# Kernel optimization log

Hardware: AMD Instinct MI355X
Metric: run time of the kernel (lower is better)

The kernel has to match this reference:

```python
import jax, jax.numpy as jnp
import numpy as np

N = 100000
E = 1600000
H = 64      # hidden_size
NH = 8      # num_heads
DH = H // NH  # per-head dim (heads are the LAST axis, as in the torch code)


def _lin(x, W, b):
    return x @ W + b


def setup_inputs() -> dict:
    key = jax.random.key(0)
    ks = jax.random.split(key, 18)
    s = 0.05
    inp = {
        "h_x": jax.random.normal(ks[0], (N, H), jnp.float32),
        "h_e": jax.random.normal(ks[1], (E, H), jnp.float32),
        "row": jax.random.randint(ks[2], (E,), 0, N, jnp.int32),  # dst node of each nonzero
        "col": jax.random.randint(ks[3], (E,), 0, N, jnp.int32),  # src node of each nonzero
    }
    names = ["q", "k", "v", "e", "oh", "oe"]
    for i, nm in enumerate(names):
        inp["W" + nm] = jax.random.normal(ks[4 + 2 * i], (H, H), jnp.float32) * s
        inp["b" + nm] = jax.random.normal(ks[5 + 2 * i], (H,), jnp.float32) * s
    return inp


def reference(h_x, h_e, row, col, Wq, bq, Wk, bk, Wv, bv, We, be, Woh, boh, Woe, boe):
    n = h_x.shape[0]
    m = h_e.shape[0]
    q = _lin(h_x, Wq, bq).reshape(n, DH, NH)
    k = _lin(h_x, Wk, bk).reshape(n, DH, NH)
    v = _lin(h_x, Wv, bv).reshape(n, DH, NH)
    e = _lin(h_e, We, be).reshape(m, DH, NH)

    # SDDMM: per-nonzero (i=row, j=col), per-head dot of q[i] and k[j]  -> (E, NH)
    scores = (q[row] * k[col]).sum(axis=1) / jnp.sqrt(jnp.float32(DH))

    # edge gating: e.sum over dh axis -> (E, NH)
    e_gate = e.sum(axis=1)
    scores = scores * e_gate

    # oe branch (uses pre-softmax gated scores)
    oe_feat = scores[:, None, :] * e          # (E, DH, NH)
    oe = _lin(oe_feat.reshape(m, H), Woe, boe)

    # sparse softmax over dim=1 (per destination row), per head
    mx = jax.ops.segment_max(scores, row, num_segments=n)      # (N, NH)
    ex = jnp.exp(scores - mx[row])
    den = jax.ops.segment_sum(ex, row, num_segments=n)         # (N, NH)
    sm = ex / den[row]                                          # (E, NH)

    # bSpMM: h_out[i,:,h] = sum_{e: row[e]=i} sm[e,h] * v[col[e],:,h]
    h_out = jax.ops.segment_sum(sm[:, None, :] * v[col], row, num_segments=n)
    oh = _lin(h_out.reshape(n, H), Woh, boh)
    return (oh, oe)
```

## Files before the change

kernel.cpp:

```cpp
#include <hip/hip_runtime.h>

typedef __attribute__((ext_vector_type(8))) short bf16x8;
typedef __attribute__((ext_vector_type(4))) float f32x4;
typedef __attribute__((ext_vector_type(16))) unsigned char u8x16;

__device__ __forceinline__ float bf2f(unsigned short h) {
  return __uint_as_float(((unsigned)h) << 16);
}
__device__ __forceinline__ unsigned cvtpk(float a, float b) {
  unsigned r;
  asm("v_cvt_pk_bf16_f32 %0, %1, %2" : "=v"(r) : "v"(a), "v"(b));
  return r;
}
__device__ __forceinline__ unsigned short f2bf(float f) {
  return (unsigned short)(cvtpk(f, f) & 0xffffu);
}
__device__ __forceinline__ bf16x8 pack8(f32x4 x0, f32x4 x1) {
  union { bf16x8 v; unsigned u[4]; } z;
  z.u[0] = cvtpk(x0[0], x0[1]);
  z.u[1] = cvtpk(x0[2], x0[3]);
  z.u[2] = cvtpk(x1[0], x1[1]);
  z.u[3] = cvtpk(x1[2], x1[3]);
  return z.v;
}

__device__ __forceinline__ int fragpos(int nb, int n15) {
  return (((nb & 1) * 2 + (n15 >> 3)) << 4) + ((nb >> 1) << 3) + (n15 & 7);
}

template<bool IN_BF16, bool OUT_BF16>
__global__ void __launch_bounds__(256) gemm64_kernel(const void* __restrict__ Ain,
    const float* __restrict__ W, const float* __restrict__ bias,
    void* __restrict__ Out, int M) {
  const int tid = threadIdx.x;
  const int l = tid & 63;
  const int g = l >> 4;
  const int n15 = l & 15;

  bf16x8 bfrag[4][2];
  float bv[4];
#pragma unroll
  for (int nb = 0; nb < 4; ++nb) {
    bv[nb] = bias[nb * 16 + n15];
#pragma unroll
    for (int kb = 0; kb < 2; ++kb)
#pragma unroll
      for (int j = 0; j < 8; ++j)
        bfrag[nb][kb][j] = (short)f2bf(W[(kb * 32 + g * 8 + j) * 64 + nb * 16 + n15]);
  }

  int wid = (blockIdx.x * blockDim.x + tid) >> 6;
  int nw = (gridDim.x * blockDim.x) >> 6;
  int ntiles = (M + 15) >> 4;
  for (int t = wid; t < ntiles; t += nw) {
    int m0 = t << 4;
    int arow = m0 + n15;
    bf16x8 a0, a1;
    if (arow < M) {
      if constexpr (IN_BF16) {
        const unsigned short* ap = (const unsigned short*)Ain + (size_t)arow * 64 + g * 8;
        a0 = *(const bf16x8*)ap;
        a1 = *(const bf16x8*)(ap + 32);
      } else {
        const float* ap = (const float*)Ain + (size_t)arow * 64 + g * 8;
        a0 = pack8(*(const f32x4*)ap, *(const f32x4*)(ap + 4));
        a1 = pack8(*(const f32x4*)(ap + 32), *(const f32x4*)(ap + 36));
      }
    } else {
#pragma unroll
      for (int j = 0; j < 8; ++j) { a0[j] = 0; a1[j] = 0; }
    }
    f32x4 acc[4];
#pragma unroll
    for (int nb = 0; nb < 4; ++nb) {
      acc[nb] = (f32x4){bv[nb], bv[nb], bv[nb], bv[nb]};
      acc[nb] = __builtin_amdgcn_mfma_f32_16x16x32_bf16(a0, bfrag[nb][0], acc[nb], 0, 0, 0);
      acc[nb] = __builtin_amdgcn_mfma_f32_16x16x32_bf16(a1, bfrag[nb][1], acc[nb], 0, 0, 0);
    }
#pragma unroll
    for (int nb = 0; nb < 4; ++nb)
#pragma unroll
      for (int r = 0; r < 4; ++r) {
        int orow = m0 + g * 4 + r;
        if (orow < M) {
          float val = acc[nb][r];
          size_t oidx = (size_t)orow * 64 + nb * 16 + n15;
          if constexpr (OUT_BF16) ((unsigned short*)Out)[oidx] = f2bf(val);
          else                    ((float*)Out)[oidx] = val;
        }
      }
  }
}

__global__ void __launch_bounds__(256) qkv3_kernel(const float* __restrict__ hx,
    const float* __restrict__ Wq, const float* __restrict__ bq,
    const float* __restrict__ Wk, const float* __restrict__ bk,
    const float* __restrict__ Wv, const float* __restrict__ bv,
    signed char* __restrict__ q8, signed char* __restrict__ k8,
    signed char* __restrict__ v8,
    float* __restrict__ sq, float* __restrict__ sk, float* __restrict__ sv, int M) {
  const int tid = threadIdx.x;
  const int l = tid & 63;
  const int g = l >> 4;
  const int n15 = l & 15;
  const float* Ws[3] = {Wq, Wk, Wv};
  const float* bs[3] = {bq, bk, bv};
  signed char* outs[3] = {q8, k8, v8};
  float* scl[3] = {sq, sk, sv};

  bf16x8 bfrag[3][4][2];
  float bvv[3][4];
#pragma unroll
  for (int w = 0; w < 3; ++w)
#pragma unroll
    for (int nb = 0; nb < 4; ++nb) {
      bvv[w][nb] = bs[w][nb * 16 + n15];
#pragma unroll
      for (int kb = 0; kb < 2; ++kb)
#pragma unroll
        for (int j = 0; j < 8; ++j)
          bfrag[w][nb][kb][j] = (short)f2bf(Ws[w][(kb * 32 + g * 8 + j) * 64 + nb * 16 + n15]);
    }

  int wid = (blockIdx.x * blockDim.x + tid) >> 6;
  int nw = (gridDim.x * blockDim.x) >> 6;
  int ntiles = (M + 15) >> 4;
  for (int t = wid; t < ntiles; t += nw) {
    int m0 = t << 4;
    int arow = m0 + n15;
    bf16x8 a0, a1;
    if (arow < M) {
      const float* ap = hx + (size_t)arow * 64 + g * 8;
      a0 = pack8(*(const f32x4*)ap, *(const f32x4*)(ap + 4));
      a1 = pack8(*(const f32x4*)(ap + 32), *(const f32x4*)(ap + 36));
    } else {
#pragma unroll
      for (int j = 0; j < 8; ++j) { a0[j] = 0; a1[j] = 0; }
    }
#pragma unroll
    for (int w = 0; w < 3; ++w) {
      f32x4 acc[4];
#pragma unroll
      for (int nb = 0; nb < 4; ++nb) {
        acc[nb] = (f32x4){bvv[w][nb], bvv[w][nb], bvv[w][nb], bvv[w][nb]};
        acc[nb] = __builtin_amdgcn_mfma_f32_16x16x32_bf16(a0, bfrag[w][nb][0], acc[nb], 0, 0, 0);
        acc[nb] = __builtin_amdgcn_mfma_f32_16x16x32_bf16(a1, bfrag[w][nb][1], acc[nb], 0, 0, 0);
      }
#pragma unroll
      for (int r = 0; r < 4; ++r) {
        float am = fmaxf(fmaxf(fabsf(acc[0][r]), fabsf(acc[1][r])),
                         fmaxf(fabsf(acc[2][r]), fabsf(acc[3][r])));
        am = fmaxf(am, __shfl_xor(am, 1, 64));
        am = fmaxf(am, __shfl_xor(am, 2, 64));
        am = fmaxf(am, __shfl_xor(am, 4, 64));
        am = fmaxf(am, __shfl_xor(am, 8, 64));
        am = fmaxf(am, 1e-10f);
        float inv = 127.0f / am;
        int orow = m0 + g * 4 + r;
        if (orow < M) {
          if (n15 == 0) scl[w][orow] = am / 127.0f;
#pragma unroll
          for (int nb = 0; nb < 4; ++nb) {
            int qi = __float2int_rn(acc[nb][r] * inv);
            int pos = (w == 2) ? (nb * 16 + n15) : fragpos(nb, n15);
            outs[w][(size_t)orow * 64 + pos] = (signed char)qi;
          }
        }
      }
    }
  }
}

__global__ void wemprep_kernel(const float* __restrict__ We, const float* __restrict__ be,
                               float* __restrict__ WeM, float* __restrict__ beM) {
  int tid = threadIdx.x;
  if (tid < 512) {
    int d = tid >> 3, h = tid & 7;
    float s = 0.f;
#pragma unroll
    for (int m = 0; m < 8; ++m) s += We[d * 64 + m * 8 + h];
    WeM[d * 8 + h] = s * 0.35355339059327373f;
  }
  if (tid < 8) {
    float s = 0.f;
#pragma unroll
    for (int m = 0; m < 8; ++m) s += be[tid + m * 8];
    beM[tid] = s * 0.35355339059327373f;
  }
}

__global__ void __launch_bounds__(256) edge_fused_kernel(
    const float* __restrict__ he,
    const int* __restrict__ rowi, const int* __restrict__ coli,
    const int* __restrict__ eslot,
    const signed char* __restrict__ q8, const signed char* __restrict__ k8,
    const float* __restrict__ sq, const float* __restrict__ sk,
    const float* __restrict__ We, const float* __restrict__ be,
    const float* __restrict__ Woe, const float* __restrict__ boe,
    const float* __restrict__ WeM, const float* __restrict__ beM,
    float* __restrict__ oe, float* __restrict__ escores, int E) {
  const int tid = threadIdx.x;
  const int wv = tid >> 6;
  const int l = tid & 63;
  const int g = l >> 4;
  const int n15 = l & 15;

  __shared__ unsigned short feat_lds[4][16 * 72];

  bf16x8 bfE[4][2], bfO[4][2];
  float beV[4], boV[4];
#pragma unroll
  for (int nb = 0; nb < 4; ++nb) {
    beV[nb] = be[nb * 16 + n15];
    boV[nb] = boe[nb * 16 + n15];
#pragma unroll
    for (int kb = 0; kb < 2; ++kb)
#pragma unroll
      for (int j = 0; j < 8; ++j) {
        bfE[nb][kb][j] = (short)f2bf(We[(kb * 32 + g * 8 + j) * 64 + nb * 16 + n15]);
        bfO[nb][kb][j] = (short)f2bf(Woe[(kb * 32 + g * 8 + j) * 64 + nb * 16 + n15]);
      }
  }
  bf16x8 gB0, gB1, mB;
  const bool hv = (n15 < 8);
#pragma unroll
  for (int j = 0; j < 8; ++j) {
    gB0[j] = hv ? (short)f2bf(WeM[(g * 8 + j) * 8 + n15]) : (short)0;
    gB1[j] = hv ? (short)f2bf(WeM[(32 + g * 8 + j) * 8 + n15]) : (short)0;
    mB[j]  = (hv && j == n15) ? (short)0x3F80 : (short)0;
  }
  const float beMv = hv ? beM[n15] : 0.f;

  const int ntiles = (E + 15) >> 4;
  int wid = (blockIdx.x * blockDim.x + tid) >> 6;
  int nw = (gridDim.x * blockDim.x) >> 6;
  for (int t = wid; t < ntiles; t += nw) {
    const int m0 = t << 4;
    const int es = min(m0 + n15, E - 1);
    const int rq = rowi[es], rc = coli[es], sl = eslot[es];

    u8x16 qv = *(const u8x16*)(q8 + (size_t)rq * 64 + g * 16);
    u8x16 kv = *(const u8x16*)(k8 + (size_t)rc * 64 + g * 16);
    const float sqk = sq[rq] * sk[rc];

    const float* ap = he + (size_t)es * 64 + g * 8;
    bf16x8 a0 = pack8(*(const f32x4*)ap, *(const f32x4*)(ap + 4));
    bf16x8 a1 = pack8(*(const f32x4*)(ap + 32), *(const f32x4*)(ap + 36));

    f32x4 acc[4];
#pragma unroll
    for (int nb = 0; nb < 4; ++nb) {
      acc[nb] = (f32x4){beV[nb], beV[nb], beV[nb], beV[nb]};
      acc[nb] = __builtin_amdgcn_mfma_f32_16x16x32_bf16(a0, bfE[nb][0], acc[nb], 0, 0, 0);
      acc[nb] = __builtin_amdgcn_mfma_f32_16x16x32_bf16(a1, bfE[nb][1], acc[nb], 0, 0, 0);
    }
    f32x4 gate = (f32x4){beMv, beMv, beMv, beMv};
    gate = __builtin_amdgcn_mfma_f32_16x16x32_bf16(a0, gB0, gate, 0, 0, 0);
    gate = __builtin_amdgcn_mfma_f32_16x16x32_bf16(a1, gB1, gate, 0, 0, 0);

    f32x4 p0a, p0b, p1a, p1b;
#pragma unroll
    for (int j = 0; j < 4; ++j) {
      p0a[j] = (float)((int)(signed char)qv[j]      * (int)(signed char)kv[j]);
      p0b[j] = (float)((int)(signed char)qv[4 + j]  * (int)(signed char)kv[4 + j]);
      p1a[j] = (float)((int)(signed char)qv[8 + j]  * (int)(signed char)kv[8 + j]);
      p1b[j] = (float)((int)(signed char)qv[12 + j] * (int)(signed char)kv[12 + j]);
    }
    bf16x8 pa0 = pack8(p0a, p0b), pa1 = pack8(p1a, p1b);
    f32x4 p = (f32x4){0.f, 0.f, 0.f, 0.f};
    p = __builtin_amdgcn_mfma_f32_16x16x32_bf16(pa0, mB, p, 0, 0, 0);
    p = __builtin_amdgcn_mfma_f32_16x16x32_bf16(pa1, mB, p, 0, 0, 0);

    float s_[4];
#pragma unroll
    for (int r = 0; r < 4; ++r)
      s_[r] = p[r] * gate[r] * __shfl(sqk, g * 4 + r, 64);
#pragma unroll
    for (int r = 0; r < 4; ++r) {
      int slot = __shfl(sl, g * 4 + r, 64);
      if (hv && m0 + g * 4 + r < E) escores[(size_t)slot * 8 + n15] = s_[r];
    }
#pragma unroll
    for (int r = 0; r < 4; ++r) {
      float o = __shfl_xor(s_[r], 8, 64);
      if (!hv) s_[r] = o;
    }
#pragma unroll
    for (int nb = 0; nb < 4; ++nb)
#pragma unroll
      for (int r = 0; r < 4; ++r)
        feat_lds[wv][(g * 4 + r) * 72 + nb * 16 + n15] = f2bf(s_[r] * acc[nb][r]);
    const unsigned short* fpt = &feat_lds[wv][n15 * 72 + g * 8];
    a0 = *(const bf16x8*)fpt;
    a1 = *(const bf16x8*)(fpt + 32);
#pragma unroll
    for (int nb = 0; nb < 4; ++nb) {
      f32x4 c2 = (f32x4){boV[nb], boV[nb], boV[nb], boV[nb]};
      c2 = __builtin_amdgcn_mfma_f32_16x16x32_bf16(a0, bfO[nb][0], c2, 0, 0, 0);
      c2 = __builtin_amdgcn_mfma_f32_16x16x32_bf16(a1, bfO[nb][1], c2, 0, 0, 0);
#pragma unroll
      for (int r = 0; r < 4; ++r) {
        int orow = m0 + g * 4 + r;
        if (orow < E) oe[(size_t)orow * 64 + nb * 16 + n15] = c2[r];
      }
    }
  }
}

__global__ void zero_kernel(int* __restrict__ p, int n) {
  int i = blockIdx.x * blockDim.x + threadIdx.x;
  if (i < n) p[i] = 0;
}

__global__ void hist_kernel(const int* __restrict__ row, int* __restrict__ deg, int E) {
  int gid = blockIdx.x * blockDim.x + threadIdx.x;
  if (gid < E) atomicAdd(&deg[row[gid]], 1);
}

#define SCAN_B 256
#define SCAN_E 8
__global__ void scan1_kernel(const int* __restrict__ deg, int* __restrict__ rowptr,
                             int* __restrict__ blksum, int n) {
  __shared__ int sh[SCAN_B];
  int base = blockIdx.x * (SCAN_B * SCAN_E) + threadIdx.x * SCAN_E;
  int v[SCAN_E];
  int s = 0;
#pragma unroll
  for (int j = 0; j < SCAN_E; ++j) {
    v[j] = (base + j < n) ? deg[base + j] : 0;
    s += v[j];
  }
  sh[threadIdx.x] = s;
  __syncthreads();
  for (int off = 1; off < SCAN_B; off <<= 1) {
    int t = (threadIdx.x >= off) ? sh[threadIdx.x - off] : 0;
    __syncthreads();
    sh[threadIdx.x] += t;
    __syncthreads();
  }
  if (threadIdx.x == SCAN_B - 1) blksum[blockIdx.x] = sh[SCAN_B - 1];
  int run = sh[threadIdx.x] - s;
#pragma unroll
  for (int j = 0; j < SCAN_E; ++j) {
    if (base + j < n) rowptr[base + j] = run;
    run += v[j];
  }
}

__global__ void scan2_kernel(int* __restrict__ blksum, int nb) {
  __shared__ int sh[SCAN_B];
  int v = (threadIdx.x < nb) ? blksum[threadIdx.x] : 0;
  sh[threadIdx.x] = v;
  __syncthreads();
  for (int off = 1; off < SCAN_B; off <<= 1) {
    int t = (threadIdx.x >= off) ? sh[threadIdx.x - off] : 0;
    __syncthreads();
    sh[threadIdx.x] += t;
    __syncthreads();
  }
  if (threadIdx.x < nb) blksum[threadIdx.x] = sh[threadIdx.x] - v;
}

__global__ void scan3_kernel(int* __restrict__ rowptr, int* __restrict__ cursor,
                             const int* __restrict__ blksum, int n) {
  int i = blockIdx.x * blockDim.x + threadIdx.x;
  if (i >= n) return;
  int v = rowptr[i] + blksum[i / (SCAN_B * SCAN_E)];
  rowptr[i] = v;
  cursor[i] = v;
}

__global__ void scatter_kernel(const int* __restrict__ row, const int* __restrict__ col,
                               int* __restrict__ cursor, int* __restrict__ eslot,
                               int* __restrict__ ecol, int E) {
  int gid = blockIdx.x * blockDim.x + threadIdx.x;
  if (gid >= E) return;
  int r = row[gid];
  int slot = atomicAdd(&cursor[r], 1);
  eslot[gid] = slot;
  ecol[slot] = col[gid];
}

__global__ void __launch_bounds__(256) row_attn_kernel(const float* __restrict__ escores,
    const int* __restrict__ rowptr, const int* __restrict__ deg,
    const int* __restrict__ ecol,
    const signed char* __restrict__ v8, const float* __restrict__ sv,
    float* __restrict__ hout, int n) {
  int gid = blockIdx.x * blockDim.x + threadIdx.x;
  int r = gid >> 6, lane = threadIdx.x & 63;
  if (r >= n) return;
  int gi = lane >> 4, j = lane & 15;
  int start = rowptr[r], dg = deg[r];

  f32x4 acc = (f32x4){0.f, 0.f, 0.f, 0.f};
  f32x4 den = (f32x4){0.f, 0.f, 0.f, 0.f};
  for (int i = gi; i < dg; i += 4) {
    int idx = start + i;
    int c = ecol[idx];
    f32x4 svec = *(const f32x4*)(escores + (size_t)idx * 8 + 4 * (j & 1));
    unsigned vvu = *(const unsigned*)(v8 + (size_t)c * 64 + j * 4);
    float scv = sv[c];
#pragma unroll
    for (int m = 0; m < 4; ++m) {
      float ex = __expf(svec[m]);
      float vm = (float)((signed char)((vvu >> (8 * m)) & 0xff));
      den[m] += ex;
      acc[m] += ex * scv * vm;
    }
  }
#pragma unroll
  for (int m = 0; m < 4; ++m) {
    acc[m] += __shfl_xor(acc[m], 16, 64);
    acc[m] += __shfl_xor(acc[m], 32, 64);
    den[m] += __shfl_xor(den[m], 16, 64);
    den[m] += __shfl_xor(den[m], 32, 64);
  }
  if (gi == 0) {
    f32x4 o;
#pragma unroll
    for (int m = 0; m < 4; ++m) o[m] = (dg > 0) ? acc[m] / den[m] : 0.f;
    *(f32x4*)(hout + (size_t)r * 64 + j * 4) = o;
  }
}

extern "C" void kernel_launch(void* const* d_in, const int* in_sizes, int n_in,
                              void* d_out, int out_size, void* d_ws, size_t ws_size,
                              hipStream_t stream) {
  const float* hx  = (const float*)d_in[0];
  const float* he  = (const float*)d_in[1];
  const int*   row = (const int*)d_in[2];
  const int*   col = (const int*)d_in[3];
  const float* Wq = (const float*)d_in[4],  *bq = (const float*)d_in[5];
  const float* Wk = (const float*)d_in[6],  *bk = (const float*)d_in[7];
  const float* Wv = (const float*)d_in[8],  *bv = (const float*)d_in[9];
  const float* We = (const float*)d_in[10], *be = (const float*)d_in[11];
  const float* Woh = (const float*)d_in[12], *boh = (const float*)d_in[13];
  const float* Woe = (const float*)d_in[14], *boe = (const float*)d_in[15];

  const int n = in_sizes[0] / 64;
  const int E = in_sizes[2];

  float* out = (float*)d_out;
  float* oh = out;
  float* oe = out + (size_t)n * 64;

  signed char* q8 = (signed char*)d_ws;
  signed char* k8 = q8 + (size_t)n * 64;
  signed char* v8 = k8 + (size_t)n * 64;
  float* sq = (float*)(v8 + (size_t)n * 64);
  float* sk = sq + n;
  float* sv = sk + n;
  float* escores = sv + n;
  float* hout    = escores + (size_t)E * 8;

  int* deg    = (int*)(hout + (size_t)n * 64);
  int* rowptr = deg + n;
  int* cursor = rowptr + n;
  int* blksum = cursor + n;
  int* eslot  = blksum + 256;
  int* ecol   = eslot + (size_t)E;
  float* WeM  = (float*)(ecol + (size_t)E);
  float* beM  = WeM + 512;

  const int nb_scan = (n + SCAN_B * SCAN_E - 1) / (SCAN_B * SCAN_E);

  zero_kernel<<<(n + 255) / 256, 256, 0, stream>>>(deg, n);
  hist_kernel<<<(E + 255) / 256, 256, 0, stream>>>(row, deg, E);
  scan1_kernel<<<nb_scan, SCAN_B, 0, stream>>>(deg, rowptr, blksum, n);
  scan2_kernel<<<1, SCAN_B, 0, stream>>>(blksum, nb_scan);
  scan3_kernel<<<(n + 255) / 256, 256, 0, stream>>>(rowptr, cursor, blksum, n);
  scatter_kernel<<<(E + 255) / 256, 256, 0, stream>>>(row, col, cursor, eslot, ecol, E);

  qkv3_kernel<<<512, 256, 0, stream>>>(hx, Wq, bq, Wk, bk, Wv, bv,
                                       q8, k8, v8, sq, sk, sv, n);
  wemprep_kernel<<<1, 512, 0, stream>>>(We, be, WeM, beM);

  edge_fused_kernel<<<2048, 256, 0, stream>>>(he, row, col, eslot, q8, k8, sq, sk,
                                              We, be, Woe, boe, WeM, beM,
                                              oe, escores, E);

  row_attn_kernel<<<(n + 3) / 4, 256, 0, stream>>>(escores, rowptr, deg, ecol,
                                                   v8, sv, hout, n);
  gemm64_kernel<false, false><<<512, 256, 0, stream>>>(hout, Woh, boh, oh, n);
}
```

Baseline: 596.3 us.

## Switch q/k/v from int8 to bf16 and software-pipeline edge gathers

Replaces per-row int8 quantization of q, k and v (with scale arrays) by plain bf16 storage. This removes the quantize reductions and scale loads but doubles the bytes gathered per edge. The edge kernel now prefetches the next tile's indices and q/k rows, two tiles ahead for indices, to hide gather latency at the cost of extra registers. The row attention loop is unrolled by two so more gather loads are in flight.

```diff
diff --git a/kernel.cpp b/kernel.cpp
--- a/kernel.cpp
+++ b/kernel.cpp
@@ -2,7 +2,7 @@
 
 typedef __attribute__((ext_vector_type(8))) short bf16x8;
 typedef __attribute__((ext_vector_type(4))) float f32x4;
-typedef __attribute__((ext_vector_type(16))) unsigned char u8x16;
+typedef __attribute__((ext_vector_type(4))) unsigned short u16x4;
 
 __device__ __forceinline__ float bf2f(unsigned short h) {
   return __uint_as_float(((unsigned)h) << 16);
@@ -22,10 +22,6 @@
   z.u[2] = cvtpk(x1[0], x1[1]);
   z.u[3] = cvtpk(x1[2], x1[3]);
   return z.v;
-}
-
-__device__ __forceinline__ int fragpos(int nb, int n15) {
-  return (((nb & 1) * 2 + (n15 >> 3)) << 4) + ((nb >> 1) << 3) + (n15 & 7);
 }
 
 template<bool IN_BF16, bool OUT_BF16>
@@ -96,17 +92,15 @@
     const float* __restrict__ Wq, const float* __restrict__ bq,
     const float* __restrict__ Wk, const float* __restrict__ bk,
     const float* __restrict__ Wv, const float* __restrict__ bv,
-    signed char* __restrict__ q8, signed char* __restrict__ k8,
-    signed char* __restrict__ v8,
-    float* __restrict__ sq, float* __restrict__ sk, float* __restrict__ sv, int M) {
+    unsigned short* __restrict__ q, unsigned short* __restrict__ k,
+    unsigned short* __restrict__ v, int M) {
   const int tid = threadIdx.x;
   const int l = tid & 63;
   const int g = l >> 4;
   const int n15 = l & 15;
   const float* Ws[3] = {Wq, Wk, Wv};
   const float* bs[3] = {bq, bk, bv};
-  signed char* outs[3] = {q8, k8, v8};
-  float* scl[3] = {sq, sk, sv};
+  unsigned short* outs[3] = {q, k, v};
 
   bf16x8 bfrag[3][4][2];
   float bvv[3][4];
@@ -147,26 +141,13 @@
         acc[nb] = __builtin_amdgcn_mfma_f32_16x16x32_bf16(a1, bfrag[w][nb][1], acc[nb], 0, 0, 0);
       }
 #pragma unroll
-      for (int r = 0; r < 4; ++r) {
-        float am = fmaxf(fmaxf(fabsf(acc[0][r]), fabsf(acc[1][r])),
-                         fmaxf(fabsf(acc[2][r]), fabsf(acc[3][r])));
-        am = fmaxf(am, __shfl_xor(am, 1, 64));
-        am = fmaxf(am, __shfl_xor(am, 2, 64));
-        am = fmaxf(am, __shfl_xor(am, 4, 64));
-        am = fmaxf(am, __shfl_xor(am, 8, 64));
-        am = fmaxf(am, 1e-10f);
-        float inv = 127.0f / am;
-        int orow = m0 + g * 4 + r;
-        if (orow < M) {
-          if (n15 == 0) scl[w][orow] = am / 127.0f;
-#pragma unroll
-          for (int nb = 0; nb < 4; ++nb) {
-            int qi = __float2int_rn(acc[nb][r] * inv);
-            int pos = (w == 2) ? (nb * 16 + n15) : fragpos(nb, n15);
-            outs[w][(size_t)orow * 64 + pos] = (signed char)qi;
-          }
+      for (int nb = 0; nb < 4; ++nb)
+#pragma unroll
+        for (int r = 0; r < 4; ++r) {
+          int orow = m0 + g * 4 + r;
+          if (orow < M)
+            outs[w][(size_t)orow * 64 + nb * 16 + n15] = f2bf(acc[nb][r]);
         }
-      }
     }
   }
 }
@@ -193,8 +174,7 @@
     const float* __restrict__ he,
     const int* __restrict__ rowi, const int* __restrict__ coli,
     const int* __restrict__ eslot,
-    const signed char* __restrict__ q8, const signed char* __restrict__ k8,
-    const float* __restrict__ sq, const float* __restrict__ sk,
+    const unsigned short* __restrict__ qb, const unsigned short* __restrict__ kbuf,
     const float* __restrict__ We, const float* __restrict__ be,
     const float* __restrict__ Woe, const float* __restrict__ boe,
     const float* __restrict__ WeM, const float* __restrict__ beM,
@@ -234,16 +214,47 @@
   const int ntiles = (E + 15) >> 4;
   int wid = (blockIdx.x * blockDim.x + tid) >> 6;
   int nw = (gridDim.x * blockDim.x) >> 6;
-  for (int t = wid; t < ntiles; t += nw) {
-    const int m0 = t << 4;
-    const int es = min(m0 + n15, E - 1);
-    const int rq = rowi[es], rc = coli[es], sl = eslot[es];
-
-    u8x16 qv = *(const u8x16*)(q8 + (size_t)rq * 64 + g * 16);
-    u8x16 kv = *(const u8x16*)(k8 + (size_t)rc * 64 + g * 16);
-    const float sqk = sq[rq] * sk[rc];
-
-    const float* ap = he + (size_t)es * 64 + g * 8;
+  if (wid >= ntiles) return;
+
+  int t0 = wid;
+  int sl0;
+  bf16x8 qv0, qv1, kv0, kv1;
+  {
+    int es = min((t0 << 4) + n15, E - 1);
+    int rq = rowi[es], rc = coli[es];
+    sl0 = eslot[es];
+    const unsigned short* qp = qb + (size_t)rq * 64 + g * 8;
+    const unsigned short* kp = kbuf + (size_t)rc * 64 + g * 8;
+    qv0 = *(const bf16x8*)qp; qv1 = *(const bf16x8*)(qp + 32);
+    kv0 = *(const bf16x8*)kp; kv1 = *(const bf16x8*)(kp + 32);
+  }
+  int t1 = t0 + nw;
+  bool more = t1 < ntiles;
+  int rq1 = 0, rc1 = 0, sl1 = 0;
+  if (more) {
+    int es = min((t1 << 4) + n15, E - 1);
+    rq1 = rowi[es]; rc1 = coli[es]; sl1 = eslot[es];
+  }
+
+  for (;;) {
+    bf16x8 nqv0 = qv0, nqv1 = qv1, nkv0 = kv0, nkv1 = kv1;
+    if (more) {
+      const unsigned short* qp = qb + (size_t)rq1 * 64 + g * 8;
+      const unsigned short* kp = kbuf + (size_t)rc1 * 64 + g * 8;
+      nqv0 = *(const bf16x8*)qp; nqv1 = *(const bf16x8*)(qp + 32);
+      nkv0 = *(const bf16x8*)kp; nkv1 = *(const bf16x8*)(kp + 32);
+    }
+    int t2 = t1 + nw;
+    bool more2 = more && (t2 < ntiles);
+    int rq2 = rq1, rc2 = rc1, sl2 = sl1;
+    if (more2) {
+      int es = min((t2 << 4) + n15, E - 1);
+      rq2 = rowi[es]; rc2 = coli[es]; sl2 = eslot[es];
+    }
+
+    const int m0 = t0 << 4;
+    const int es0 = min(m0 + n15, E - 1);
+    const float* ap = he + (size_t)es0 * 64 + g * 8;
     bf16x8 a0 = pack8(*(const f32x4*)ap, *(const f32x4*)(ap + 4));
     bf16x8 a1 = pack8(*(const f32x4*)(ap + 32), *(const f32x4*)(ap + 36));
 
@@ -261,10 +272,10 @@
     f32x4 p0a, p0b, p1a, p1b;
 #pragma unroll
     for (int j = 0; j < 4; ++j) {
-      p0a[j] = (float)((int)(signed char)qv[j]      * (int)(signed char)kv[j]);
-      p0b[j] = (float)((int)(signed char)qv[4 + j]  * (int)(signed char)kv[4 + j]);
-      p1a[j] = (float)((int)(signed char)qv[8 + j]  * (int)(signed char)kv[8 + j]);
-      p1b[j] = (float)((int)(signed char)qv[12 + j] * (int)(signed char)kv[12 + j]);
+      p0a[j] = bf2f((unsigned short)qv0[j]) * bf2f((unsigned short)kv0[j]);
+      p0b[j] = bf2f((unsigned short)qv0[4 + j]) * bf2f((unsigned short)kv0[4 + j]);
+      p1a[j] = bf2f((unsigned short)qv1[j]) * bf2f((unsigned short)kv1[j]);
+      p1b[j] = bf2f((unsigned short)qv1[4 + j]) * bf2f((unsigned short)kv1[4 + j]);
     }
     bf16x8 pa0 = pack8(p0a, p0b), pa1 = pack8(p1a, p1b);
     f32x4 p = (f32x4){0.f, 0.f, 0.f, 0.f};
@@ -273,11 +284,10 @@
 
     float s_[4];
 #pragma unroll
-    for (int r = 0; r < 4; ++r)
-      s_[r] = p[r] * gate[r] * __shfl(sqk, g * 4 + r, 64);
+    for (int r = 0; r < 4; ++r) s_[r] = p[r] * gate[r];
 #pragma unroll
     for (int r = 0; r < 4; ++r) {
-      int slot = __shfl(sl, g * 4 + r, 64);
+      int slot = __shfl(sl0, g * 4 + r, 64);
       if (hv && m0 + g * 4 + r < E) escores[(size_t)slot * 8 + n15] = s_[r];
     }
 #pragma unroll
@@ -304,6 +314,12 @@
         if (orow < E) oe[(size_t)orow * 64 + nb * 16 + n15] = c2[r];
       }
     }
+
+    if (!more) break;
+    t0 = t1; sl0 = sl1;
+    qv0 = nqv0; qv1 = nqv1; kv0 = nkv0; kv1 = nkv1;
+    t1 = t2; rq1 = rq2; rc1 = rc2; sl1 = sl2;
+    more = more2;
   }
 }
 
@@ -384,8 +400,7 @@
 __global__ void __launch_bounds__(256) row_attn_kernel(const float* __restrict__ escores,
     const int* __restrict__ rowptr, const int* __restrict__ deg,
     const int* __restrict__ ecol,
-    const signed char* __restrict__ v8, const float* __restrict__ sv,
-    float* __restrict__ hout, int n) {
+    const unsigned short* __restrict__ vb, float* __restrict__ hout, int n) {
   int gid = blockIdx.x * blockDim.x + threadIdx.x;
   int r = gid >> 6, lane = threadIdx.x & 63;
   if (r >= n) return;
@@ -394,18 +409,32 @@
 
   f32x4 acc = (f32x4){0.f, 0.f, 0.f, 0.f};
   f32x4 den = (f32x4){0.f, 0.f, 0.f, 0.f};
-  for (int i = gi; i < dg; i += 4) {
+  int i = gi;
+  for (; i + 4 < dg; i += 8) {
+    int ia = start + i, ib = start + i + 4;
+    int ca = ecol[ia], cb = ecol[ib];
+    f32x4 sa = *(const f32x4*)(escores + (size_t)ia * 8 + 4 * (j & 1));
+    f32x4 sb = *(const f32x4*)(escores + (size_t)ib * 8 + 4 * (j & 1));
+    u16x4 va = *(const u16x4*)(vb + (size_t)ca * 64 + j * 4);
+    u16x4 vc = *(const u16x4*)(vb + (size_t)cb * 64 + j * 4);
+#pragma unroll
+    for (int m = 0; m < 4; ++m) {
+      float ea = __expf(sa[m]);
+      float eb = __expf(sb[m]);
+      den[m] += ea + eb;
+      acc[m] += ea * bf2f(va[m]) + eb * bf2f(vc[m]);
+    }
+  }
+  if (i < dg) {
     int idx = start + i;
     int c = ecol[idx];
-    f32x4 svec = *(const f32x4*)(escores + (size_t)idx * 8 + 4 * (j & 1));
-    unsigned vvu = *(const unsigned*)(v8 + (size_t)c * 64 + j * 4);
-    float scv = sv[c];
+    f32x4 sv = *(const f32x4*)(escores + (size_t)idx * 8 + 4 * (j & 1));
+    u16x4 vv = *(const u16x4*)(vb + (size_t)c * 64 + j * 4);
 #pragma unroll
     for (int m = 0; m < 4; ++m) {
-      float ex = __expf(svec[m]);
-      float vm = (float)((signed char)((vvu >> (8 * m)) & 0xff));
+      float ex = __expf(sv[m]);
       den[m] += ex;
-      acc[m] += ex * scv * vm;
+      acc[m] += ex * bf2f(vv[m]);
     }
   }
 #pragma unroll
@@ -444,13 +473,10 @@
   float* oh = out;
   float* oe = out + (size_t)n * 64;
 
-  signed char* q8 = (signed char*)d_ws;
-  signed char* k8 = q8 + (size_t)n * 64;
-  signed char* v8 = k8 + (size_t)n * 64;
-  float* sq = (float*)(v8 + (size_t)n * 64);
-  float* sk = sq + n;
-  float* sv = sk + n;
-  float* escores = sv + n;
+  unsigned short* qb   = (unsigned short*)d_ws;
+  unsigned short* kb   = qb + (size_t)n * 64;
+  unsigned short* vbuf = kb + (size_t)n * 64;
+  float* escores = (float*)(vbuf + (size_t)n * 64);
   float* hout    = escores + (size_t)E * 8;
 
   int* deg    = (int*)(hout + (size_t)n * 64);
@@ -471,15 +497,14 @@
   scan3_kernel<<<(n + 255) / 256, 256, 0, stream>>>(rowptr, cursor, blksum, n);
   scatter_kernel<<<(E + 255) / 256, 256, 0, stream>>>(row, col, cursor, eslot, ecol, E);
 
-  qkv3_kernel<<<512, 256, 0, stream>>>(hx, Wq, bq, Wk, bk, Wv, bv,
-                                       q8, k8, v8, sq, sk, sv, n);
+  qkv3_kernel<<<512, 256, 0, stream>>>(hx, Wq, bq, Wk, bk, Wv, bv, qb, kb, vbuf, n);
   wemprep_kernel<<<1, 512, 0, stream>>>(We, be, WeM, beM);
 
-  edge_fused_kernel<<<2048, 256, 0, stream>>>(he, row, col, eslot, q8, k8, sq, sk,
+  edge_fused_kernel<<<2048, 256, 0, stream>>>(he, row, col, eslot, qb, kb,
                                               We, be, Woe, boe, WeM, beM,
                                               oe, escores, E);
 
   row_attn_kernel<<<(n + 3) / 4, 256, 0, stream>>>(escores, rowptr, deg, ecol,
-                                                   v8, sv, hout, n);
+                                                   vbuf, hout, n);
   gemm64_kernel<false, false><<<512, 256, 0, stream>>>(hout, Woh, boh, oh, n);
 }
```

Result: faster. 525.0 us, median of 2 (-12.0%).
